# Kernel optimization log

Hardware: AMD Instinct MI355X
Metric: run time of the kernel (lower is better)

## Reference

```python
import math
import jax, jax.numpy as jnp
import numpy as np

TOP_K = 2
N_EXP = 8
CAP_FACTOR = 1.25  # train_capacity (module in training mode)
MIN_CAP = 4


def setup_inputs() -> dict:
    key = jax.random.key(0)
    k1, k2 = jax.random.split(key)
    x = jax.random.normal(k1, (8192, 1024), dtype=jnp.float32)
    w_g = jax.random.normal(k2, (8, 1024), dtype=jnp.float32) * 0.02  # Linear(n_embd, n_experts) weight [E, C]
    return {"x": x, "w_g": w_g}


def _capacity(num_tokens: int) -> int:
    cap = math.floor(TOP_K * CAP_FACTOR * num_tokens / N_EXP)
    cap += cap % 2
    return max(cap, MIN_CAP)


def reference(x, w_g):
    N = x.shape[0]
    capacity = _capacity(N)  # static Python int

    logits = x @ w_g.T  # [N, E]
    topk_vals, topk_idx = jax.lax.top_k(logits, TOP_K)  # [N, k]

    # softmax over only the top-k logits (others -inf)
    rows = jnp.arange(N)[:, None]
    masked = jnp.full_like(logits, -jnp.inf).at[rows, topk_idx].set(topk_vals)
    router_probs = jax.nn.softmax(masked, axis=-1)  # [N, E]

    # one-hot expert assignment, priority-ordered: [k, N, E]
    exp_mask = jnp.transpose(jax.nn.one_hot(topk_idx, N_EXP, dtype=jnp.int32), (1, 0, 2))

    # position-in-expert rank via cumsum over flattened (k*N) priority order
    exp_rank = jnp.cumsum(exp_mask.reshape(TOP_K * N, N_EXP), axis=0) - 1
    exp_rank = exp_rank.reshape(TOP_K, N, N_EXP)

    # drop tokens exceeding capacity
    exp_mask = exp_mask * (exp_rank < capacity).astype(jnp.int32)
    used_capacity = jnp.sum(exp_mask, axis=(0, 1))  # [E]

    rank = jnp.sum(exp_mask * exp_rank, axis=-1)  # [k, N] slot index per assignment
    exp_weights = exp_mask.astype(router_probs.dtype) * router_probs[None]  # [k, N, E]
    rank_sc = jax.nn.one_hot(rank, capacity, dtype=router_probs.dtype)  # [k, N, cap]

    cb_weight = jnp.einsum('kne,knc->nec', exp_weights, rank_sc)  # [N, E, cap]
    sec_mask = cb_weight.astype(bool)
    return used_capacity, cb_weight, sec_mask
```

## Files before the change

### kernel.cpp

```cpp
#include <hip/hip_runtime.h>
#include <math.h>

#define N_TOK 8192
#define C_DIM 1024
#define NEXP 8
#define CAP 2560
#define NASSIGN (2 * N_TOK)

__global__ __launch_bounds__(256) void gate_kernel(const float* __restrict__ x,
                                                   const float* __restrict__ wg,
                                                   int* __restrict__ epair,
                                                   float* __restrict__ p1o,
                                                   float* __restrict__ p2o) {
    __shared__ float4 wls[NEXP * 256];
    const int tid = threadIdx.x;
    const float4* wg4 = (const float4*)wg;
    for (int i = tid; i < NEXP * 256; i += 256) wls[i] = wg4[i];
    __syncthreads();

    const int wave = tid >> 6;
    const int lane = tid & 63;
    const int n = blockIdx.x * 4 + wave;
    const float4* x4 = (const float4*)(x + (size_t)n * C_DIM);

    double acc[NEXP];
#pragma unroll
    for (int e = 0; e < NEXP; ++e) acc[e] = 0.0;

#pragma unroll
    for (int c = 0; c < 4; ++c) {
        float4 xv = x4[c * 64 + lane];
#pragma unroll
        for (int e = 0; e < NEXP; ++e) {
            float4 wv = wls[e * 256 + c * 64 + lane];
            acc[e] = fma((double)xv.x, (double)wv.x, acc[e]);
            acc[e] = fma((double)xv.y, (double)wv.y, acc[e]);
            acc[e] = fma((double)xv.z, (double)wv.z, acc[e]);
            acc[e] = fma((double)xv.w, (double)wv.w, acc[e]);
        }
    }

#pragma unroll
    for (int off = 32; off >= 1; off >>= 1) {
#pragma unroll
        for (int e = 0; e < NEXP; ++e) acc[e] += __shfl_xor(acc[e], off);
    }

    if (lane == 0) {
        double v1 = -1e300, v2 = -1e300;
        int i1 = 0, i2 = 0;
#pragma unroll
        for (int e = 0; e < NEXP; ++e) {
            double v = acc[e];
            if (v > v1) { v2 = v1; i2 = i1; v1 = v; i1 = e; }
            else if (v > v2) { v2 = v; i2 = e; }
        }
        double z = exp(v2 - v1);
        double inv = 1.0 / (1.0 + z);
        epair[n] = i1 | (i2 << 8);
        p1o[n] = (float)inv;
        p2o[n] = (float)(z * inv);
    }
}

__global__ __launch_bounds__(1024) void scan_kernel(const int* __restrict__ epair,
                                                    int* __restrict__ rank,
                                                    float* __restrict__ used_cap) {
    __shared__ unsigned long long slo[1024];
    __shared__ unsigned long long shi[1024];
    const int t = threadIdx.x;

    int evals[16];
    unsigned long long lo = 0, hi = 0;
#pragma unroll
    for (int j = 0; j < 16; ++j) {
        int i = t * 16 + j;
        int n = i & (N_TOK - 1);
        int pr = epair[n];
        int e = (i >= N_TOK) ? ((pr >> 8) & 0xff) : (pr & 0xff);
        evals[j] = e;
        unsigned long long inc = 1ULL << (16 * (e & 3));
        if (e < 4) lo += inc; else hi += inc;
    }
    slo[t] = lo;
    shi[t] = hi;
    __syncthreads();

    for (int d = 1; d < 1024; d <<= 1) {
        unsigned long long alo = 0, ahi = 0;
        if (t >= d) { alo = slo[t - d]; ahi = shi[t - d]; }
        __syncthreads();
        if (t >= d) { slo[t] += alo; shi[t] += ahi; }
        __syncthreads();
    }

    unsigned long long rlo = (t > 0) ? slo[t - 1] : 0ULL;
    unsigned long long rhi = (t > 0) ? shi[t - 1] : 0ULL;
#pragma unroll
    for (int j = 0; j < 16; ++j) {
        int e = evals[j];
        int sh = 16 * (e & 3);
        int r = (int)(((e < 4 ? rlo : rhi) >> sh) & 0xffff);
        rank[t * 16 + j] = r;
        if (e < 4) rlo += 1ULL << sh; else rhi += 1ULL << sh;
    }

    if (t == 1023) {
        unsigned long long tlo = slo[1023], thi = shi[1023];
#pragma unroll
        for (int e = 0; e < NEXP; ++e) {
            int c = (int)(((e < 4 ? tlo : thi) >> (16 * (e & 3))) & 0xffff);
            used_cap[e] = (float)(c < CAP ? c : CAP);
        }
    }
}

__global__ __launch_bounds__(256) void scatter_kernel(const int* __restrict__ epair,
                                                      const float* __restrict__ p1,
                                                      const float* __restrict__ p2,
                                                      const int* __restrict__ rank,
                                                      float* __restrict__ cb,
                                                      float* __restrict__ mask) {
    int i = blockIdx.x * 256 + threadIdx.x;
    if (i >= NASSIGN) return;
    int n = i & (N_TOK - 1);
    int pr = epair[n];
    int r = rank[i];
    int e;
    float p;
    if (i >= N_TOK) { e = (pr >> 8) & 0xff; p = p2[n]; }
    else            { e = pr & 0xff;        p = p1[n]; }
    if (r < CAP) {
        size_t idx = (size_t)n * (NEXP * CAP) + (size_t)e * CAP + (size_t)r;
        cb[idx]   = p;
        mask[idx] = 1.0f;
    }
}

extern "C" void kernel_launch(void* const* d_in, const int* in_sizes, int n_in,
                              void* d_out, int out_size, void* d_ws, size_t ws_size,
                              hipStream_t stream) {
    const float* x  = (const float*)d_in[0];
    const float* wg = (const float*)d_in[1];

    float* out  = (float*)d_out;
    float* used = out;
    float* cb   = out + NEXP;
    float* mask = cb + (size_t)N_TOK * NEXP * CAP;

    int*   epair = (int*)d_ws;
    float* p1    = (float*)d_ws + N_TOK;
    float* p2    = (float*)d_ws + 2 * N_TOK;
    int*   rank  = (int*)d_ws + 3 * N_TOK;

    hipMemsetAsync(d_out, 0, (size_t)out_size * sizeof(float), stream);

    gate_kernel<<<N_TOK / 4, 256, 0, stream>>>(x, wg, epair, p1, p2);
    scan_kernel<<<1, 1024, 0, stream>>>(epair, rank, used);
    scatter_kernel<<<(NASSIGN + 255) / 256, 256, 0, stream>>>(epair, p1, p2, rank, cb, mask);
}
```

Before: 1.301 ms.

## Fuse output zero-fill with scatter in per-token kernel, drop memset

Removes the full-output hipMemsetAsync and instead has one block per token zero its [E, cap] slice of both outputs with float4 stores, sync, then write the two routed entries. This aims to avoid writing the huge output once in the memset and then touching it again in a separate scatter launch. The used_capacity slot is no longer memset, but scan_kernel writes all of it. The risk is that a per-block fill at this output size is store-bandwidth bound and may be no faster than the driver memset.

```diff
diff --git a/kernel.cpp b/kernel.cpp
--- a/kernel.cpp
+++ b/kernel.cpp
@@ -115,25 +115,42 @@
     }
 }
 
-__global__ __launch_bounds__(256) void scatter_kernel(const int* __restrict__ epair,
-                                                      const float* __restrict__ p1,
-                                                      const float* __restrict__ p2,
-                                                      const int* __restrict__ rank,
-                                                      float* __restrict__ cb,
-                                                      float* __restrict__ mask) {
-    int i = blockIdx.x * 256 + threadIdx.x;
-    if (i >= NASSIGN) return;
-    int n = i & (N_TOK - 1);
-    int pr = epair[n];
-    int r = rank[i];
-    int e;
-    float p;
-    if (i >= N_TOK) { e = (pr >> 8) & 0xff; p = p2[n]; }
-    else            { e = pr & 0xff;        p = p1[n]; }
-    if (r < CAP) {
-        size_t idx = (size_t)n * (NEXP * CAP) + (size_t)e * CAP + (size_t)r;
-        cb[idx]   = p;
-        mask[idx] = 1.0f;
+__global__ __launch_bounds__(256) void fill_scatter_kernel(const int* __restrict__ epair,
+                                                           const float* __restrict__ p1,
+                                                           const float* __restrict__ p2,
+                                                           const int* __restrict__ rank,
+                                                           float* __restrict__ cb,
+                                                           float* __restrict__ mask) {
+    const int n = blockIdx.x;
+    const size_t row = (size_t)n * (NEXP * CAP);
+    float4* cb4 = (float4*)(cb + row);
+    float4* mk4 = (float4*)(mask + row);
+    const float4 z = make_float4(0.f, 0.f, 0.f, 0.f);
+
+#pragma unroll
+    for (int it = 0; it < (NEXP * CAP / 4) / 256; ++it) {
+        int i = it * 256 + threadIdx.x;
+        cb4[i] = z;
+        mk4[i] = z;
+    }
+    __syncthreads();
+
+    if (threadIdx.x == 0) {
+        int pr = epair[n];
+        int e1 = pr & 0xff;
+        int e2 = (pr >> 8) & 0xff;
+        int r1 = rank[n];
+        int r2 = rank[N_TOK + n];
+        if (r1 < CAP) {
+            int t = e1 * CAP + r1;
+            cb[row + t] = p1[n];
+            mask[row + t] = 1.0f;
+        }
+        if (r2 < CAP) {
+            int t = e2 * CAP + r2;
+            cb[row + t] = p2[n];
+            mask[row + t] = 1.0f;
+        }
     }
 }
 
@@ -153,9 +170,7 @@
     float* p2    = (float*)d_ws + 2 * N_TOK;
     int*   rank  = (int*)d_ws + 3 * N_TOK;
 
-    hipMemsetAsync(d_out, 0, (size_t)out_size * sizeof(float), stream);
-
     gate_kernel<<<N_TOK / 4, 256, 0, stream>>>(x, wg, epair, p1, p2);
     scan_kernel<<<1, 1024, 0, stream>>>(epair, rank, used);
-    scatter_kernel<<<(NASSIGN + 255) / 256, 256, 0, stream>>>(epair, p1, p2, rank, cb, mask);
+    fill_scatter_kernel<<<N_TOK, 256, 0, stream>>>(epair, p1, p2, rank, cb, mask);
 }
```

New measurement: 1.357 ms. +4.3%, slower.

## Fuse output zero-fill and scatter into one dense float4 write kernel

Applied to the files above, without the earlier changes.

Drops the full-output memset and the sparse scatter kernel. A single dense kernel now writes every element of the combine-weight and mask tensors, using float4 stores, and computes nonzeros in place from the per-token expert, rank and probability. This removes the separate scatter pass and the extra kernel launch, though the same ~1.3 GB of output still has to be written. The used_capacity entries are still written by the scan kernel and are no longer zeroed first, which is fine because the scan writes all of them.

```diff
diff --git a/kernel.cpp b/kernel.cpp
--- a/kernel.cpp
+++ b/kernel.cpp
@@ -6,6 +6,7 @@
 #define NEXP 8
 #define CAP 2560
 #define NASSIGN (2 * N_TOK)
+#define ROW_F4 (NEXP * CAP / 4)
 
 __global__ __launch_bounds__(256) void gate_kernel(const float* __restrict__ x,
                                                    const float* __restrict__ wg,
@@ -115,26 +116,46 @@
     }
 }
 
-__global__ __launch_bounds__(256) void scatter_kernel(const int* __restrict__ epair,
-                                                      const float* __restrict__ p1,
-                                                      const float* __restrict__ p2,
-                                                      const int* __restrict__ rank,
-                                                      float* __restrict__ cb,
-                                                      float* __restrict__ mask) {
-    int i = blockIdx.x * 256 + threadIdx.x;
-    if (i >= NASSIGN) return;
-    int n = i & (N_TOK - 1);
-    int pr = epair[n];
-    int r = rank[i];
-    int e;
-    float p;
-    if (i >= N_TOK) { e = (pr >> 8) & 0xff; p = p2[n]; }
-    else            { e = pr & 0xff;        p = p1[n]; }
-    if (r < CAP) {
-        size_t idx = (size_t)n * (NEXP * CAP) + (size_t)e * CAP + (size_t)r;
-        cb[idx]   = p;
-        mask[idx] = 1.0f;
+__global__ __launch_bounds__(256) void out_kernel(const int* __restrict__ epair,
+                                                  const float* __restrict__ p1,
+                                                  const float* __restrict__ p2,
+                                                  const int* __restrict__ rank,
+                                                  float* __restrict__ cb,
+                                                  float* __restrict__ mask) {
+    const int n = blockIdx.y;
+    const int i = blockIdx.x * 256 + threadIdx.x;
+    const int e = i / 640;
+    const int c0 = (i - e * 640) * 4;
+
+    const int pr = epair[n];
+    const int e1 = pr & 0xff;
+    const int e2 = (pr >> 8) & 0xff;
+    const int r1 = rank[n];
+    const int r2 = rank[N_TOK + n];
+    const float pv1 = p1[n];
+    const float pv2 = p2[n];
+
+    float4 cbv = make_float4(0.f, 0.f, 0.f, 0.f);
+    float4 mkv = make_float4(0.f, 0.f, 0.f, 0.f);
+    const bool a1 = (e == e1), a2 = (e == e2);
+    if (a1 | a2) {
+#pragma unroll
+        for (int j = 0; j < 4; ++j) {
+            const int c = c0 + j;
+            const bool m1 = a1 && (r1 == c);
+            const bool m2 = a2 && (r2 == c);
+            const float cv = m1 ? pv1 : (m2 ? pv2 : 0.f);
+            const float mv = (m1 | m2) ? 1.f : 0.f;
+            if (j == 0) { cbv.x = cv; mkv.x = mv; }
+            if (j == 1) { cbv.y = cv; mkv.y = mv; }
+            if (j == 2) { cbv.z = cv; mkv.z = mv; }
+            if (j == 3) { cbv.w = cv; mkv.w = mv; }
+        }
     }
+
+    const size_t base = (size_t)n * ROW_F4 + i;
+    ((float4*)cb)[base] = cbv;
+    ((float4*)mask)[base] = mkv;
 }
 
 extern "C" void kernel_launch(void* const* d_in, const int* in_sizes, int n_in,
@@ -153,9 +174,7 @@
     float* p2    = (float*)d_ws + 2 * N_TOK;
     int*   rank  = (int*)d_ws + 3 * N_TOK;
 
-    hipMemsetAsync(d_out, 0, (size_t)out_size * sizeof(float), stream);
-
     gate_kernel<<<N_TOK / 4, 256, 0, stream>>>(x, wg, epair, p1, p2);
     scan_kernel<<<1, 1024, 0, stream>>>(epair, rank, used);
-    scatter_kernel<<<(NASSIGN + 255) / 256, 256, 0, stream>>>(epair, p1, p2, rank, cb, mask);
+    out_kernel<<<dim3(ROW_F4 / 256, N_TOK), 256, 0, stream>>>(epair, p1, p2, rank, cb, mask);
 }
```

After: 1.369 ms. 5.2% more time.
